# Kernel tuning notes

Measured on AMD Instinct MI355X. Metric: run time of the kernel, lower is better.

## Reference

```python
import jax, jax.numpy as jnp
import numpy as np

EPS = 1e-5  # LayerNorm eps (torch default)
K_NN = 16   # matches init kwarg k


def _knn_idx(pos, k):
    # pos: (B,N,3) -> (B,N,k) indices of k nearest points (sorted by distance,
    # includes self at slot 0), matching pytorch3d knn_points(return_sorted=True).
    sq = jnp.sum(pos * pos, axis=-1)                                   # (B,N)
    d2 = sq[:, :, None] + sq[:, None, :] - 2.0 * jnp.einsum('bnd,bmd->bnm', pos, pos)
    _, idx = jax.lax.top_k(-d2, k)                                     # ascending distance
    return idx


def _gather(feats, idx):
    # feats: (B,N,C), idx: (B,N,K) -> (B,N,K,C)
    return jax.vmap(lambda f, i: f[i])(feats, idx)


def _ln(x, g, b):
    mu = jnp.mean(x, axis=-1, keepdims=True)
    var = jnp.mean((x - mu) ** 2, axis=-1, keepdims=True)
    return (x - mu) * jax.lax.rsqrt(var + EPS) * g + b


def setup_inputs() -> dict:
    key = jax.random.key(0)
    B, N, D, H = 2, 4096, 128, 12
    ks = jax.random.split(key, 16)
    s = 0.05
    f32 = jnp.float32
    return {
        'x': jax.random.normal(ks[0], (B, N, D), f32),
        'pos': jax.random.normal(ks[1], (B, N, 3), f32),
        # linear projections (bias=False)
        'w_q': jax.random.normal(ks[2], (D, D), f32) * s,
        'w_k': jax.random.normal(ks[3], (D, D), f32) * s,
        'w_v': jax.random.normal(ks[4], (D, D), f32) * s,
        # pos_mlp: Linear(3,H) -> LN(H) -> ReLU -> Linear(H,D)
        'pos_w1': jax.random.normal(ks[5], (H, 3), f32) * s,
        'pos_b1': jnp.zeros((H,), f32),
        'pos_g': jnp.ones((H,), f32),
        'pos_beta': jnp.zeros((H,), f32),
        'pos_w2': jax.random.normal(ks[6], (D, H), f32) * s,
        'pos_b2': jnp.zeros((D,), f32),
        # attn_mlp: Linear(D,D) -> LN(D) -> ReLU -> Linear(D,D)
        'attn_w1': jax.random.normal(ks[7], (D, D), f32) * s,
        'attn_b1': jnp.zeros((D,), f32),
        'attn_g': jnp.ones((D,), f32),
        'attn_beta': jnp.zeros((D,), f32),
        'attn_w2': jax.random.normal(ks[8], (D, D), f32) * s,
        'attn_b2': jnp.zeros((D,), f32),
    }


def reference(x, pos, w_q, w_k, w_v,
              pos_w1, pos_b1, pos_g, pos_beta, pos_w2, pos_b2,
              attn_w1, attn_b1, attn_g, attn_beta, attn_w2, attn_b2):
    idx = _knn_idx(pos, K_NN)                        # (B,N,K)
    q = x @ w_q.T                                    # (B,N,D)
    kf = _gather(x @ w_k.T, idx)                     # (B,N,K,D)
    vf = _gather(x @ w_v.T, idx)                     # (B,N,K,D)
    pos_rel = pos[:, :, None, :] - _gather(pos, idx)  # (B,N,K,3)
    # pos_mlp
    pe = _ln(pos_rel @ pos_w1.T + pos_b1, pos_g, pos_beta)
    pe = jax.nn.relu(pe) @ pos_w2.T + pos_b2         # (B,N,K,D)
    # attn_mlp on (q - k + pos_enc)
    w = q[:, :, None, :] - kf + pe
    w = _ln(w @ attn_w1.T + attn_b1, attn_g, attn_beta)
    w = jax.nn.relu(w) @ attn_w2.T + attn_b2         # (B,N,K,D)
    attn = jax.nn.softmax(w, axis=2)                 # softmax over neighbor dim
    return jnp.einsum('bnkd,bnkd->bnd', attn, vf + pe)
```

## Files before the change

kernel.cpp:

```cpp
#include <hip/hip_runtime.h>
#include <hip/hip_bf16.h>
#include <math.h>

#define BATCH 2
#define NPTS 4096
#define DIM 128
#define HID 12
#define KNN 16
#define NSLOT 24

#define KNN_BLOCKS (BATCH * NPTS / 4)
#define FOLD_BLOCKS 128
#define PACK_BLOCKS 5

typedef __attribute__((ext_vector_type(8))) short short8;
typedef __attribute__((ext_vector_type(4))) float f32x4;

__device__ __forceinline__ short f2b(float f) {
  unsigned u = __float_as_uint(f);
  unsigned r = (u + 0x7fffu + ((u >> 16) & 1u)) >> 16;
  return (short)r;
}
__device__ __forceinline__ float b2f(short h) {
  return __uint_as_float(((unsigned)(unsigned short)h) << 16);
}

#define KNN_EVENTS(d2v, base, odd)                                        \
  {                                                                       \
    unsigned long long mask_ = __ballot((d2v) < thr);                     \
    while (mask_) {                                                       \
      const int src_ = (int)__builtin_ctzll(mask_);                       \
      mask_ &= mask_ - 1;                                                 \
      const float dc_ = __shfl((d2v), src_);                              \
      const int ic_ = (base) + 2 * src_ + (odd);                          \
      const float vup_ = __shfl_up(vald, 1);                              \
      const int iup_ = __shfl_up(validx, 1);                              \
      const bool less_ = dc_ < vald;                                      \
      const bool take_ = less_ && (lane == 0 || dc_ >= vup_);             \
      if (is_slot) {                                                      \
        if (take_) { vald = dc_; validx = ic_; }                          \
        else if (less_) { vald = vup_; validx = iup_; }                   \
      }                                                                   \
    }                                                                     \
    const float v15_ = __shfl(vald, 15);                                  \
    thr = v15_ + v15_ * 1e-5f;                                            \
  }

__device__ void knn_body(int bid, const float* __restrict__ pos,
                         int* __restrict__ knn_out) {
  const int t = threadIdx.x;
  const int w = t >> 6;
  const int lane = t & 63;
  const int n = (bid << 2) + w;
  const int b = n >> 12;
  const int qn = n & (NPTS - 1);

  const float* pb = pos + b * NPTS * 3;
  const float qx = pb[qn * 3 + 0];
  const float qy = pb[qn * 3 + 1];
  const float qz = pb[qn * 3 + 2];

  float d2a, d2b;
  {
    const float2* pp = (const float2*)(pb + lane * 6);
    const float2 u0 = pp[0], u1 = pp[1], u2 = pp[2];
    float dx = qx - u0.x, dy = qy - u0.y, dz = qz - u1.x;
    d2a = fmaf(dx, dx, fmaf(dy, dy, dz * dz));
    dx = qx - u1.y; dy = qy - u2.x; dz = qz - u2.y;
    d2b = fmaf(dx, dx, fmaf(dy, dy, dz * dz));
  }
  float v = d2a;
  int vi = lane * 2;
#pragma unroll
  for (int k = 2; k <= 64; k <<= 1) {
#pragma unroll
    for (int j = k >> 1; j >= 1; j >>= 1) {
      const float ov = __shfl_xor(v, j);
      const int oi = __shfl_xor(vi, j);
      const bool up = ((lane & k) == 0);
      const bool lowpos = ((lane & j) == 0);
      const bool keep_min = (lowpos == up);
      const bool take = keep_min ? (ov < v) : (ov > v);
      if (take) { v = ov; vi = oi; }
    }
  }

  const bool is_slot = (lane < NSLOT);
  float vald = is_slot ? v : __builtin_inff();
  int validx = is_slot ? vi : -1;
  const float v15i = __shfl(v, 15);
  float thr = v15i + v15i * 1e-5f;

  KNN_EVENTS(d2b, 0, 1)

#pragma unroll 1
  for (int it = 1; it < NPTS / 128; ++it) {
    const float2* pp = (const float2*)(pb + it * 384 + lane * 6);
    const float2 u0 = pp[0], u1 = pp[1], u2 = pp[2];
    float dx = qx - u0.x, dy = qy - u0.y, dz = qz - u1.x;
    const float e2a = fmaf(dx, dx, fmaf(dy, dy, dz * dz));
    dx = qx - u1.y; dy = qy - u2.x; dz = qz - u2.y;
    const float e2b = fmaf(dx, dx, fmaf(dy, dy, dz * dz));
    KNN_EVENTS(e2a, it * 128, 0)
    KNN_EVENTS(e2b, it * 128, 1)
  }

  double d2e = 1e300;
  if (is_slot) {
    const double ex = (double)qx - (double)pb[validx * 3 + 0];
    const double ey = (double)qy - (double)pb[validx * 3 + 1];
    const double ez = (double)qz - (double)pb[validx * 3 + 2];
    d2e = ex * ex + ey * ey + ez * ez;
  }
  int rank = 0;
#pragma unroll 1
  for (int j = 0; j < NSLOT; ++j) {
    const double dj = __shfl(d2e, j);
    const int ij = __shfl(validx, j);
    if (dj < d2e || (dj == d2e && ij < validx)) ++rank;
  }
  if (is_slot && rank < KNN) knn_out[((b << 12) + qn) * KNN + rank] = validx;
}

__device__ void fold_body(int bid, const float* __restrict__ aw1,
                          const float* __restrict__ wq, const float* __restrict__ wk,
                          short* __restrict__ WqaHi, short* __restrict__ WqaLo,
                          short* __restrict__ WkaHi, short* __restrict__ WkaLo) {
  const float* w = (bid < 64) ? wq : wk;
  short* oh = (bid < 64) ? WqaHi : WkaHi;
  short* ol = (bid < 64) ? WqaLo : WkaLo;
  const int row = ((bid & 63) << 1) + (threadIdx.x >> 7);
  const int i = threadIdx.x & 127;
  float acc = 0.f;
  for (int j = 0; j < 128; ++j) acc = fmaf(aw1[row * 128 + j], w[j * 128 + i], acc);
  const short h = f2b(acc);
  oh[row * 128 + i] = h;
  ol[row * 128 + i] = f2b(acc - b2f(h));
}

__device__ void pack_body(int bid, const float* __restrict__ aw1,
                          const float* __restrict__ pw2, const float* __restrict__ pb2,
                          const float* __restrict__ ab1, const float* __restrict__ aw2,
                          const float* __restrict__ wv,
                          short* __restrict__ M1b, short* __restrict__ pw2b,
                          short* __restrict__ aw2b, float* __restrict__ c1,
                          short* __restrict__ WvHi, short* __restrict__ WvLo) {
  const int t = threadIdx.x;
  if (bid == 0) {
    const int o = t >> 1, half = t & 1;
    for (int kk = 0; kk < 16; ++kk) {
      const int k = half * 16 + kk;
      float v = 0.f;
      if (k < HID)
        for (int j = 0; j < 128; ++j) v = fmaf(aw1[o * 128 + j], pw2[j * HID + k], v);
      M1b[o * 32 + k] = (k < HID) ? f2b(v) : (short)0;
    }
    if (t < 128) {
      float v = ab1[t];
      for (int j = 0; j < 128; ++j) v = fmaf(aw1[t * 128 + j], pb2[j], v);
      c1[t] = v;
    }
  } else if (bid == 1) {
    for (int i = t; i < 128 * 32; i += 256) {
      const int o = i >> 5, k = i & 31;
      pw2b[i] = (k < HID) ? f2b(pw2[o * HID + k]) : (short)0;
    }
  } else if (bid < 4) {
    const int base = (bid - 2) * 8192;
    for (int i = t; i < 8192; i += 256) aw2b[base + i] = f2b(aw2[base + i]);
  } else {
    for (int i = t; i < 128 * 128; i += 256) {
      const float v = wv[i];
      const short h = f2b(v);
      WvHi[i] = h;
      WvLo[i] = f2b(v - b2f(h));
    }
  }
}

__global__ __launch_bounds__(256) void knn_prep_kernel(
    const float* __restrict__ pos, int* __restrict__ knn_out,
    const float* __restrict__ aw1, const float* __restrict__ wq,
    const float* __restrict__ wk,
    short* __restrict__ WqaHi, short* __restrict__ WqaLo,
    short* __restrict__ WkaHi, short* __restrict__ WkaLo,
    const float* __restrict__ pw2, const float* __restrict__ pb2,
    const float* __restrict__ ab1, const float* __restrict__ aw2,
    const float* __restrict__ wv,
    short* __restrict__ M1b, short* __restrict__ pw2b, short* __restrict__ aw2b,
    float* __restrict__ c1, short* __restrict__ WvHi, short* __restrict__ WvLo) {
  const int bid = blockIdx.x;
  if (bid < KNN_BLOCKS) {
    knn_body(bid, pos, knn_out);
  } else if (bid < KNN_BLOCKS + FOLD_BLOCKS) {
    fold_body(bid - KNN_BLOCKS, aw1, wq, wk, WqaHi, WqaLo, WkaHi, WkaLo);
  } else {
    pack_body(bid - KNN_BLOCKS - FOLD_BLOCKS, aw1, pw2, pb2, ab1, aw2, wv, M1b,
              pw2b, aw2b, c1, WvHi, WvLo);
  }
}

__global__ __launch_bounds__(256) void proj_mfma_kernel(
    const float* __restrict__ x,
    const short* __restrict__ WqaHi, const short* __restrict__ WqaLo,
    const short* __restrict__ WkaHi, const short* __restrict__ WkaLo,
    const short* __restrict__ WvHi, const short* __restrict__ WvLo,
    float* __restrict__ QA, float* __restrict__ KA, float* __restrict__ Vp) {
  const int t = threadIdx.x;
  const int wid = t >> 6, lane = t & 63;
  const int r16 = lane & 15, g4 = lane >> 4;
  const int rowbase = blockIdx.x * 32 + (wid >> 1) * 16;
  const int ch = wid & 1;

  short8 ahi[4], alo[4];
#pragma unroll
  for (int ks = 0; ks < 4; ++ks) {
    const float* xp = x + (rowbase + r16) * DIM + ks * 32 + g4 * 8;
#pragma unroll
    for (int e = 0; e < 8; ++e) {
      const float v = xp[e];
      const short h = f2b(v);
      ahi[ks][e] = h;
      alo[ks][e] = f2b(v - b2f(h));
    }
  }

  const f32x4 zero4 = {0.f, 0.f, 0.f, 0.f};
  const short* WH[3] = {WqaHi, WkaHi, WvHi};
  const short* WL[3] = {WqaLo, WkaLo, WvLo};
  float* OUT[3] = {QA, KA, Vp};
#pragma unroll
  for (int mi = 0; mi < 3; ++mi) {
    const short* wh = WH[mi];
    const short* wl = WL[mi];
    float* o = OUT[mi];
#pragma unroll
    for (int q = 0; q < 4; ++q) {
      const int col = (ch * 4 + q) * 16 + r16;
      f32x4 a = zero4;
#pragma unroll
      for (int ks = 0; ks < 4; ++ks) {
        const short8 bh = *(const short8*)(wh + col * DIM + ks * 32 + g4 * 8);
        const short8 bl = *(const short8*)(wl + col * DIM + ks * 32 + g4 * 8);
        a = __builtin_amdgcn_mfma_f32_16x16x32_bf16(ahi[ks], bh, a, 0, 0, 0);
        a = __builtin_amdgcn_mfma_f32_16x16x32_bf16(alo[ks], bh, a, 0, 0, 0);
        a = __builtin_amdgcn_mfma_f32_16x16x32_bf16(ahi[ks], bl, a, 0, 0, 0);
      }
#pragma unroll
      for (int reg = 0; reg < 4; ++reg)
        o[(rowbase + g4 * 4 + reg) * DIM + (ch * 4 + q) * 16 + r16] = a[reg];
    }
  }
}

__global__ __launch_bounds__(256) void pt_wave_kernel(
    const float* __restrict__ pos, const int* __restrict__ knn_in,
    const float* __restrict__ QA, const float* __restrict__ KA, const float* __restrict__ Vp,
    const float* __restrict__ pw1, const float* __restrict__ pb1,
    const float* __restrict__ pg, const float* __restrict__ pbeta,
    const float* __restrict__ pb2,
    const float* __restrict__ ag, const float* __restrict__ abeta,
    const float* __restrict__ ab2, const float* __restrict__ c1,
    const short* __restrict__ M1b, const short* __restrict__ pw2b,
    const short* __restrict__ aw2b,
    float* __restrict__ out) {
  __shared__ __align__(16) short z_s[2048];
  __shared__ float red_s[2][4][16];

  const int t = threadIdx.x;
  const int wid = t >> 6;
  const int lane = t & 63;
  const int r16 = lane & 15;
  const int g4 = lane >> 4;
  const int n = blockIdx.x;
  const int b = n >> 12;

  const int jA = knn_in[n * KNN + r16];
  int jC[4];
#pragma unroll
  for (int reg = 0; reg < 4; ++reg) jC[reg] = knn_in[n * KNN + g4 * 4 + reg];

  const float qx = pos[n * 3 + 0], qy = pos[n * 3 + 1], qz = pos[n * 3 + 2];
  const int ja_g = b * NPTS + jA;
  const float rx = qx - pos[ja_g * 3 + 0];
  const float ry = qy - pos[ja_g * 3 + 1];
  const float rz = qz - pos[ja_g * 3 + 2];

  float hr[HID];
  {
    float mu = 0.f;
#pragma unroll
    for (int hh = 0; hh < HID; ++hh) {
      const float v = pb1[hh] + rx * pw1[hh * 3 + 0] + ry * pw1[hh * 3 + 1] +
                      rz * pw1[hh * 3 + 2];
      hr[hh] = v;
      mu += v;
    }
    mu *= (1.f / HID);
    float var = 0.f;
#pragma unroll
    for (int hh = 0; hh < HID; ++hh) { const float d = hr[hh] - mu; var = fmaf(d, d, var); }
    const float rs = rsqrtf(var * (1.f / HID) + 1e-5f);
#pragma unroll
    for (int hh = 0; hh < HID; ++hh)
      hr[hh] = fmaxf(fmaf((hr[hh] - mu) * rs, pg[hh], pbeta[hh]), 0.f);
  }

  short8 a1 = {0, 0, 0, 0, 0, 0, 0, 0};
  if (g4 == 0) {
#pragma unroll
    for (int e = 0; e < 8; ++e) a1[e] = f2b(hr[e]);
  } else if (g4 == 1) {
#pragma unroll
    for (int e = 0; e < 4; ++e) a1[e] = f2b(hr[8 + e]);
  }

  const f32x4 zero4 = {0.f, 0.f, 0.f, 0.f};
  f32x4 accw[2], accp[2];
#pragma unroll
  for (int q = 0; q < 2; ++q) {
    const int boff = ((wid * 2 + q) * 16 + r16) * 32 + g4 * 8;
    const short8 bm = *(const short8*)(M1b + boff);
    const short8 bp = *(const short8*)(pw2b + boff);
    accw[q] = __builtin_amdgcn_mfma_f32_16x16x32_bf16(a1, bm, zero4, 0, 0, 0);
    accp[q] = __builtin_amdgcn_mfma_f32_16x16x32_bf16(a1, bp, zero4, 0, 0, 0);
  }

  float w1v[2][4];
#pragma unroll
  for (int q = 0; q < 2; ++q) {
    const int o = (wid * 2 + q) * 16 + r16;
    const float base = QA[n * DIM + o] + c1[o];
#pragma unroll
    for (int reg = 0; reg < 4; ++reg) {
      const float ka = KA[(b * NPTS + jC[reg]) * DIM + o];
      w1v[q][reg] = accw[q][reg] + base - ka;
    }
  }

  {
    float ps[4], pq2[4];
#pragma unroll
    for (int reg = 0; reg < 4; ++reg) {
      ps[reg] = w1v[0][reg] + w1v[1][reg];
      pq2[reg] = fmaf(w1v[0][reg], w1v[0][reg], w1v[1][reg] * w1v[1][reg]);
    }
#pragma unroll
    for (int reg = 0; reg < 4; ++reg) {
#pragma unroll
      for (int off = 1; off <= 8; off <<= 1) {
        ps[reg] += __shfl_xor(ps[reg], off);
        pq2[reg] += __shfl_xor(pq2[reg], off);
      }
    }
    if (r16 == 0) {
#pragma unroll
      for (int reg = 0; reg < 4; ++reg) {
        red_s[0][wid][g4 * 4 + reg] = ps[reg];
        red_s[1][wid][g4 * 4 + reg] = pq2[reg];
      }
    }
  }
  __syncthreads();
  float mu[4], rs[4];
#pragma unroll
  for (int reg = 0; reg < 4; ++reg) {
    const int rr = g4 * 4 + reg;
    const float s = red_s[0][0][rr] + red_s[0][1][rr] + red_s[0][2][rr] + red_s[0][3][rr];
    const float q2 = red_s[1][0][rr] + red_s[1][1][rr] + red_s[1][2][rr] + red_s[1][3][rr];
    mu[reg] = s * (1.f / 128.f);
    const float var = q2 * (1.f / 128.f) - mu[reg] * mu[reg];
    rs[reg] = rsqrtf(var + 1e-5f);
  }

  {
    char* zb = (char*)z_s;
#pragma unroll
    for (int q = 0; q < 2; ++q) {
      const int o = (wid * 2 + q) * 16 + r16;
      const float gam = ag[o], bet = abeta[o];
#pragma unroll
      for (int reg = 0; reg < 4; ++reg) {
        const int rr = g4 * 4 + reg;
        const float zv = fmaxf(fmaf((w1v[q][reg] - mu[reg]) * rs[reg], gam, bet), 0.f);
        unsigned byte = (unsigned)(rr * 256 + o * 2);
        byte ^= ((unsigned)(rr & 7) << 4) ^ ((unsigned)(rr & 8) << 2);
        *(short*)(zb + byte) = f2b(zv);
      }
    }
  }
  __syncthreads();

  short8 a2[4];
  {
    const char* zb = (const char*)z_s;
#pragma unroll
    for (int ks = 0; ks < 4; ++ks) {
      unsigned byte = (unsigned)(r16 * 256 + ks * 64 + g4 * 16);
      byte ^= ((unsigned)(r16 & 7) << 4) ^ ((unsigned)(r16 & 8) << 2);
      a2[ks] = *(const short8*)(zb + byte);
    }
  }

  f32x4 acc2[2] = {zero4, zero4};
#pragma unroll
  for (int q = 0; q < 2; ++q) {
#pragma unroll
    for (int ks = 0; ks < 4; ++ks) {
      const short8 bw =
          *(const short8*)(aw2b + ((wid * 2 + q) * 16 + r16) * DIM + ks * 32 + g4 * 8);
      acc2[q] = __builtin_amdgcn_mfma_f32_16x16x32_bf16(a2[ks], bw, acc2[q], 0, 0, 0);
    }
  }

  float ew[2][4], inv[2];
#pragma unroll
  for (int q = 0; q < 2; ++q) {
    const float bb = ab2[(wid * 2 + q) * 16 + r16];
#pragma unroll
    for (int reg = 0; reg < 4; ++reg) ew[q][reg] = acc2[q][reg] + bb;
    float m = fmaxf(fmaxf(ew[q][0], ew[q][1]), fmaxf(ew[q][2], ew[q][3]));
    m = fmaxf(m, __shfl_xor(m, 16));
    m = fmaxf(m, __shfl_xor(m, 32));
    float s = 0.f;
#pragma unroll
    for (int reg = 0; reg < 4; ++reg) { ew[q][reg] = __expf(ew[q][reg] - m); s += ew[q][reg]; }
    s += __shfl_xor(s, 16);
    s += __shfl_xor(s, 32);
    inv[q] = 1.f / s;
  }

  float o_acc[2];
#pragma unroll
  for (int q = 0; q < 2; ++q) {
    const int o = (wid * 2 + q) * 16 + r16;
    const float pb = pb2[o];
    float acc = 0.f;
#pragma unroll
    for (int reg = 0; reg < 4; ++reg) {
      const float vv = Vp[(b * NPTS + jC[reg]) * DIM + o];
      acc = fmaf(ew[q][reg] * inv[q], vv + accp[q][reg] + pb, acc);
    }
    acc += __shfl_xor(acc, 16);
    acc += __shfl_xor(acc, 32);
    o_acc[q] = acc;
  }
  if (g4 < 2) out[n * DIM + (wid * 2 + g4) * 16 + r16] = o_acc[g4];
}

extern "C" void kernel_launch(void* const* d_in, const int* in_sizes, int n_in,
                              void* d_out, int out_size, void* d_ws, size_t ws_size,
                              hipStream_t stream) {
  const float* x   = (const float*)d_in[0];
  const float* pos = (const float*)d_in[1];
  const float* wq  = (const float*)d_in[2];
  const float* wk  = (const float*)d_in[3];
  const float* wv  = (const float*)d_in[4];
  const float* pw1 = (const float*)d_in[5];
  const float* pb1 = (const float*)d_in[6];
  const float* pg  = (const float*)d_in[7];
  const float* pbt = (const float*)d_in[8];
  const float* pw2 = (const float*)d_in[9];
  const float* pb2 = (const float*)d_in[10];
  const float* aw1 = (const float*)d_in[11];
  const float* ab1 = (const float*)d_in[12];
  const float* ag  = (const float*)d_in[13];
  const float* abt = (const float*)d_in[14];
  const float* aw2 = (const float*)d_in[15];
  const float* ab2 = (const float*)d_in[16];
  float* out = (float*)d_out;

  char* ws = (char*)d_ws;
  int*   knn   = (int*)ws;
  short* WqaHi = (short*)(ws + 512u * 1024u);
  short* WqaLo = (short*)(ws + 544u * 1024u);
  short* WkaHi = (short*)(ws + 576u * 1024u);
  short* WkaLo = (short*)(ws + 608u * 1024u);
  short* M1b   = (short*)(ws + 640u * 1024u);
  short* pw2b  = (short*)(ws + 648u * 1024u);
  short* aw2b  = (short*)(ws + 656u * 1024u);
  float* c1    = (float*)(ws + 688u * 1024u);
  short* WvHi  = (short*)(ws + 704u * 1024u);
  short* WvLo  = (short*)(ws + 736u * 1024u);
  float* QA    = (float*)(ws + (1u << 20));
  float* KA    = (float*)(ws + 5u * (1u << 20));
  float* Vp    = (float*)(ws + 9u * (1u << 20));

  knn_prep_kernel<<<KNN_BLOCKS + FOLD_BLOCKS + PACK_BLOCKS, 256, 0, stream>>>(
      pos, knn, aw1, wq, wk, WqaHi, WqaLo, WkaHi, WkaLo, pw2, pb2, ab1, aw2, wv,
      M1b, pw2b, aw2b, c1, WvHi, WvLo);
  proj_mfma_kernel<<<BATCH * NPTS / 32, 256, 0, stream>>>(
      x, WqaHi, WqaLo, WkaHi, WkaLo, WvHi, WvLo, QA, KA, Vp);
  pt_wave_kernel<<<BATCH * NPTS, 256, 0, stream>>>(
      pos, knn, QA, KA, Vp, pw1, pb1, pg, pbt, pb2, ag, abt, ab2, c1, M1b, pw2b, aw2b, out);
}
```

Measured before the change: 140.3 us.

## Buffer KNN candidates in LDS and merge in batches via bitonic sort

```diff
diff --git a/kernel.cpp b/kernel.cpp
--- a/kernel.cpp
+++ b/kernel.cpp
@@ -8,6 +8,8 @@
 #define HID 12
 #define KNN 16
 #define NSLOT 24
+#define BCAP 192
+#define BCT 64
 
 #define KNN_BLOCKS (BATCH * NPTS / 4)
 #define FOLD_BLOCKS 128
@@ -25,29 +27,27 @@
   return __uint_as_float(((unsigned)(unsigned short)h) << 16);
 }
 
-#define KNN_EVENTS(d2v, base, odd)                                        \
-  {                                                                       \
-    unsigned long long mask_ = __ballot((d2v) < thr);                     \
-    while (mask_) {                                                       \
-      const int src_ = (int)__builtin_ctzll(mask_);                       \
-      mask_ &= mask_ - 1;                                                 \
-      const float dc_ = __shfl((d2v), src_);                              \
-      const int ic_ = (base) + 2 * src_ + (odd);                          \
-      const float vup_ = __shfl_up(vald, 1);                              \
-      const int iup_ = __shfl_up(validx, 1);                              \
-      const bool less_ = dc_ < vald;                                      \
-      const bool take_ = less_ && (lane == 0 || dc_ >= vup_);             \
-      if (is_slot) {                                                      \
-        if (take_) { vald = dc_; validx = ic_; }                          \
-        else if (less_) { vald = vup_; validx = iup_; }                   \
-      }                                                                   \
-    }                                                                     \
-    const float v15_ = __shfl(vald, 15);                                  \
-    thr = v15_ + v15_ * 1e-5f;                                            \
+#define BITONIC64(v, vi)                                                     \
+  {                                                                          \
+    _Pragma("unroll") for (int k_ = 2; k_ <= 64; k_ <<= 1) {                 \
+      _Pragma("unroll") for (int j_ = k_ >> 1; j_ >= 1; j_ >>= 1) {          \
+        const float ov_ = __shfl_xor((v), j_);                               \
+        const int oi_ = __shfl_xor((vi), j_);                                \
+        const bool up_ = ((lane & k_) == 0);                                 \
+        const bool lowpos_ = ((lane & j_) == 0);                             \
+        const bool keep_min_ = (lowpos_ == up_);                             \
+        const bool lt_ = (ov_ < (v)) || (ov_ == (v) && oi_ < (vi));          \
+        const bool take_ = keep_min_ ? lt_ : !lt_;                           \
+        if (take_) { (v) = ov_; (vi) = oi_; }                                \
+      }                                                                      \
+    }                                                                        \
   }
 
 __device__ void knn_body(int bid, const float* __restrict__ pos,
                          int* __restrict__ knn_out) {
+  __shared__ float bd_s[4][BCAP];
+  __shared__ int bi_s[4][BCAP];
+
   const int t = threadIdx.x;
   const int w = t >> 6;
   const int lane = t & 63;
@@ -55,54 +55,113 @@
   const int b = n >> 12;
   const int qn = n & (NPTS - 1);
 
+  float* bdl = &bd_s[w][0];
+  int* bil = &bi_s[w][0];
+
   const float* pb = pos + b * NPTS * 3;
   const float qx = pb[qn * 3 + 0];
   const float qy = pb[qn * 3 + 1];
   const float qz = pb[qn * 3 + 2];
 
-  float d2a, d2b;
+  const bool is_slot = (lane < NSLOT);
+  float vald, thr;
+  int validx;
+  int bcount = 0;
+
   {
     const float2* pp = (const float2*)(pb + lane * 6);
     const float2 u0 = pp[0], u1 = pp[1], u2 = pp[2];
     float dx = qx - u0.x, dy = qy - u0.y, dz = qz - u1.x;
-    d2a = fmaf(dx, dx, fmaf(dy, dy, dz * dz));
+    float v = fmaf(dx, dx, fmaf(dy, dy, dz * dz));
+    int vi = lane * 2;
     dx = qx - u1.y; dy = qy - u2.x; dz = qz - u2.y;
-    d2b = fmaf(dx, dx, fmaf(dy, dy, dz * dz));
-  }
-  float v = d2a;
-  int vi = lane * 2;
-#pragma unroll
-  for (int k = 2; k <= 64; k <<= 1) {
-#pragma unroll
-    for (int j = k >> 1; j >= 1; j >>= 1) {
-      const float ov = __shfl_xor(v, j);
-      const int oi = __shfl_xor(vi, j);
-      const bool up = ((lane & k) == 0);
-      const bool lowpos = ((lane & j) == 0);
-      const bool keep_min = (lowpos == up);
-      const bool take = keep_min ? (ov < v) : (ov > v);
-      if (take) { v = ov; vi = oi; }
-    }
-  }
-
-  const bool is_slot = (lane < NSLOT);
-  float vald = is_slot ? v : __builtin_inff();
-  int validx = is_slot ? vi : -1;
-  const float v15i = __shfl(v, 15);
-  float thr = v15i + v15i * 1e-5f;
-
-  KNN_EVENTS(d2b, 0, 1)
+    const float d2b = fmaf(dx, dx, fmaf(dy, dy, dz * dz));
+
+    BITONIC64(v, vi)
+    vald = is_slot ? v : __builtin_inff();
+    validx = is_slot ? vi : 0x7fffffff;
+    const float v15 = __shfl(v, 15);
+    thr = v15 + v15 * 1e-5f;
+
+    const unsigned long long m = __ballot(d2b < thr);
+    if (m) {
+      const unsigned lt = __builtin_amdgcn_mbcnt_hi(
+          (unsigned)(m >> 32), __builtin_amdgcn_mbcnt_lo((unsigned)m, 0u));
+      if (d2b < thr) { bdl[lt] = d2b; bil[lt] = 2 * lane + 1; }
+      bcount = (int)__builtin_popcountll(m);
+    }
+  }
+
+  const float2* pp = (const float2*)(pb + 384 + lane * 6);
+  float2 A0 = pp[0], A1 = pp[1], A2 = pp[2];
+  pp = (const float2*)(pb + 768 + lane * 6);
+  float2 B0 = pp[0], B1 = pp[1], B2 = pp[2];
 
 #pragma unroll 1
   for (int it = 1; it < NPTS / 128; ++it) {
-    const float2* pp = (const float2*)(pb + it * 384 + lane * 6);
-    const float2 u0 = pp[0], u1 = pp[1], u2 = pp[2];
-    float dx = qx - u0.x, dy = qy - u0.y, dz = qz - u1.x;
+    const float2 c0 = A0, c1 = A1, c2 = A2;
+    A0 = B0; A1 = B1; A2 = B2;
+    if (it + 2 < NPTS / 128) {
+      pp = (const float2*)(pb + (it + 2) * 384 + lane * 6);
+      B0 = pp[0]; B1 = pp[1]; B2 = pp[2];
+    }
+    float dx = qx - c0.x, dy = qy - c0.y, dz = qz - c1.x;
     const float e2a = fmaf(dx, dx, fmaf(dy, dy, dz * dz));
-    dx = qx - u1.y; dy = qy - u2.x; dz = qz - u2.y;
+    dx = qx - c1.y; dy = qy - c2.x; dz = qz - c2.y;
     const float e2b = fmaf(dx, dx, fmaf(dy, dy, dz * dz));
-    KNN_EVENTS(e2a, it * 128, 0)
-    KNN_EVENTS(e2b, it * 128, 1)
+
+    if (bcount >= BCT) {
+#pragma unroll 1
+      while (bcount > 0) {
+        const int take = bcount < 40 ? bcount : 40;
+        float mv = __builtin_inff();
+        int mi = 0x7fffffff;
+        if (lane < NSLOT) { mv = vald; mi = validx; }
+        else if (lane - NSLOT < take) {
+          mv = bdl[bcount - take + lane - NSLOT];
+          mi = bil[bcount - take + lane - NSLOT];
+        }
+        BITONIC64(mv, mi)
+        if (is_slot) { vald = mv; validx = mi; }
+        bcount -= take;
+      }
+      const float v15 = __shfl(vald, 15);
+      thr = v15 + v15 * 1e-5f;
+    }
+
+    {
+      const unsigned long long m = __ballot(e2a < thr);
+      if (m) {
+        const unsigned lt = __builtin_amdgcn_mbcnt_hi(
+            (unsigned)(m >> 32), __builtin_amdgcn_mbcnt_lo((unsigned)m, 0u));
+        if (e2a < thr) { bdl[bcount + lt] = e2a; bil[bcount + lt] = it * 128 + 2 * lane; }
+        bcount += (int)__builtin_popcountll(m);
+      }
+    }
+    {
+      const unsigned long long m = __ballot(e2b < thr);
+      if (m) {
+        const unsigned lt = __builtin_amdgcn_mbcnt_hi(
+            (unsigned)(m >> 32), __builtin_amdgcn_mbcnt_lo((unsigned)m, 0u));
+        if (e2b < thr) { bdl[bcount + lt] = e2b; bil[bcount + lt] = it * 128 + 2 * lane + 1; }
+        bcount += (int)__builtin_popcountll(m);
+      }
+    }
+  }
+
+#pragma unroll 1
+  while (bcount > 0) {
+    const int take = bcount < 40 ? bcount : 40;
+    float mv = __builtin_inff();
+    int mi = 0x7fffffff;
+    if (lane < NSLOT) { mv = vald; mi = validx; }
+    else if (lane - NSLOT < take) {
+      mv = bdl[bcount - take + lane - NSLOT];
+      mi = bil[bcount - take + lane - NSLOT];
+    }
+    BITONIC64(mv, mi)
+    if (is_slot) { vald = mv; validx = mi; }
+    bcount -= take;
   }
 
   double d2e = 1e300;
```

After: 140.7 us. No clear change (+0.3%).
